# Performance work log

Hardware: AMD Instinct MI355X
Metric: run time of the kernel (lower is better)

## Reference

```python
import jax, jax.numpy as jnp
import numpy as np

B, XD, ZD, XE, H, NH = 8192, 4096, 1024, 64, 128, 4
NUM_STEPS, STEP, NOISE = 10, 0.01, 1.0
EPS = 1e-5


def setup_inputs() -> dict:
    key = jax.random.key(0)
    ks = jax.random.split(key, 16)
    w = lambda k, s: jax.random.normal(k, s, jnp.float32) * 0.02
    inp = {"x": jax.random.normal(ks[0], (B, XD), jnp.float32)}
    inp.update(
        px_W1=w(ks[1], (H, ZD)), px_b1=jnp.zeros(H, jnp.float32),
        px_W2=w(ks[2], (XD, H)), px_b2=jnp.zeros(XD, jnp.float32),
        emb_W=w(ks[3], (XE, XD)), emb_b=jnp.zeros(XE, jnp.float32),
        xp_W=w(ks[4], (H, XE)), xp_b=jnp.zeros(H, jnp.float32),
        zp_W=w(ks[5], (H, ZD)), zp_b=jnp.zeros(H, jnp.float32),
        sa_Wqkv=w(ks[6], (3 * H, H)), sa_bqkv=jnp.zeros(3 * H, jnp.float32),
        sa_Wo=w(ks[7], (H, H)), sa_bo=jnp.zeros(H, jnp.float32),
        ca_Wqkv=w(ks[8], (3 * H, H)), ca_bqkv=jnp.zeros(3 * H, jnp.float32),
        ca_Wo=w(ks[9], (H, H)), ca_bo=jnp.zeros(H, jnp.float32),
        ffn_W1=w(ks[10], (H, H)), ffn_b1=jnp.zeros(H, jnp.float32),
        ffn_W2=w(ks[11], (H, H)), ffn_b2=jnp.zeros(H, jnp.float32),
        ln1_g=jnp.ones(H, jnp.float32), ln1_b=jnp.zeros(H, jnp.float32),
        ln2_g=jnp.ones(H, jnp.float32), ln2_b=jnp.zeros(H, jnp.float32),
        ln3_g=jnp.ones(H, jnp.float32), ln3_b=jnp.zeros(H, jnp.float32),
        out_W=w(ks[12], (1, H)), out_b=jnp.zeros(1, jnp.float32),
    )
    return inp


def _ln(x, g, b):
    m = jnp.mean(x, -1, keepdims=True)
    v = jnp.var(x, -1, keepdims=True)
    return (x - m) * jax.lax.rsqrt(v + EPS) * g + b


def _mha(q, k, v, Wqkv, bqkv, Wo, bo):
    # torch nn.MultiheadAttention math, batch-first layout (B, S, E)
    E = q.shape[-1]
    d = E // NH
    Wq, Wk, Wv = jnp.split(Wqkv, 3, 0)
    bq, bk, bv = jnp.split(bqkv, 3, 0)
    hd = lambda t, W, bb: (t @ W.T + bb).reshape(t.shape[0], t.shape[1], NH, d)
    qh, kh, vh = hd(q, Wq, bq), hd(k, Wk, bk), hd(v, Wv, bv)
    s = jnp.einsum('bqhd,bkhd->bhqk', qh, kh) / jnp.sqrt(jnp.float32(d))
    a = jax.nn.softmax(s, -1)
    o = jnp.einsum('bhqk,bkhd->bqhd', a, vh).reshape(q.shape[0], q.shape[1], E)
    return o @ Wo.T + bo


def _forward(x, px_W1, px_b1, px_W2, px_b2, emb_W, emb_b, xp_W, xp_b, zp_W, zp_b,
             sa_Wqkv, sa_bqkv, sa_Wo, sa_bo, ca_Wqkv, ca_bqkv, ca_Wo, ca_bo,
             ffn_W1, ffn_b1, ffn_W2, ffn_b2, ln1_g, ln1_b, ln2_g, ln2_b,
             ln3_g, ln3_b, out_W, out_b):
    bsz = x.shape[0]
    px = lambda z: jax.nn.relu(z @ px_W1.T + px_b1) @ px_W2.T + px_b2
    grad_fn = jax.grad(lambda z: jnp.sum((px(z) - x) ** 2))
    ks = jax.random.split(jax.random.key(42), NUM_STEPS + 1)
    z0 = jax.random.normal(ks[0], (bsz, ZD), jnp.float32)

    def step(z, k):
        z = z - 0.5 * STEP * grad_fn(z)
        z = z + NOISE * jnp.sqrt(jnp.float32(STEP)) * jax.random.normal(k, z.shape, z.dtype)
        return z, None

    z, _ = jax.lax.scan(step, z0, ks[1:])
    z = jax.lax.stop_gradient(z)  # torch: z.detach()

    x_recon = px(z)                               # (B, XD)
    x_tok = (x @ emb_W.T + emb_b)[:, None, :]     # (B, 1, XE)
    z_lat = z[:, None, :]                         # (B, 1, ZD)
    x_h = x_tok @ xp_W.T + xp_b                   # (B, 1, H)
    z_h = z_lat @ zp_W.T + zp_b                   # (B, 1, H)
    sa = _mha(x_h, x_h, x_h, sa_Wqkv, sa_bqkv, sa_Wo, sa_bo)
    h1 = _ln(x_h + sa, ln1_g, ln1_b)
    ca = _mha(h1, z_h, z_h, ca_Wqkv, ca_bqkv, ca_Wo, ca_bo)
    h2 = _ln(h1 + ca, ln2_g, ln2_b)
    ff = jax.nn.relu(h2 @ ffn_W1.T + ffn_b1) @ ffn_W2.T + ffn_b2
    h3 = _ln(h2 + ff, ln3_g, ln3_b)
    y_pred = h3 @ out_W.T + out_b                 # (B, 1, 1)
    return x_recon, y_pred


def reference(x, px_W1, px_b1, px_W2, px_b2, emb_W, emb_b, xp_W, xp_b, zp_W, zp_b,
              sa_Wqkv, sa_bqkv, sa_Wo, sa_bo, ca_Wqkv, ca_bqkv, ca_Wo, ca_bo,
              ffn_W1, ffn_b1, ffn_W2, ffn_b2, ln1_g, ln1_b, ln2_g, ln2_b,
              ln3_g, ln3_b, out_W, out_b):
    return _forward(x, px_W1, px_b1, px_W2, px_b2, emb_W, emb_b, xp_W, xp_b,
                    zp_W, zp_b, sa_Wqkv, sa_bqkv, sa_Wo, sa_bo, ca_Wqkv,
                    ca_bqkv, ca_Wo, ca_bo, ffn_W1, ffn_b1, ffn_W2, ffn_b2,
                    ln1_g, ln1_b, ln2_g, ln2_b, ln3_g, ln3_b, out_W, out_b)
```

## Files before the change

kernel.cpp:

```cpp
#include <hip/hip_runtime.h>
#include <hip/hip_bf16.h>
#include <cstdint>
#include <cstddef>
#include <cmath>

#define B_     8192
#define XD_    4096
#define ZD_    1024
#define XE_    64
#define H_     128
#define ZN_    (B_*ZD_)

typedef __attribute__((ext_vector_type(8))) short short8_t;
typedef __attribute__((ext_vector_type(4))) float f32x4_t;
#define MFMA16(a,b,c) __builtin_amdgcn_mfma_f32_16x16x32_bf16((a),(b),(c),0,0,0)

__host__ __device__ __forceinline__ uint32_t rotl32_(uint32_t x, int r){
#ifdef __HIP_DEVICE_COMPILE__
  return __builtin_rotateleft32(x, (uint32_t)r);
#else
  return (x<<r)|(x>>(32-r));
#endif
}

__host__ __device__ __forceinline__ void tf2x32(uint32_t k0, uint32_t k1,
                                                uint32_t x0, uint32_t x1,
                                                uint32_t* o0, uint32_t* o1){
  uint32_t k2 = k0 ^ k1 ^ 0x1BD11BDAu;
  x0 += k0; x1 += k1;
  x0 += x1; x1 = rotl32_(x1,13); x1 ^= x0;
  x0 += x1; x1 = rotl32_(x1,15); x1 ^= x0;
  x0 += x1; x1 = rotl32_(x1,26); x1 ^= x0;
  x0 += x1; x1 = rotl32_(x1, 6); x1 ^= x0;
  x0 += k1; x1 += k2 + 1u;
  x0 += x1; x1 = rotl32_(x1,17); x1 ^= x0;
  x0 += x1; x1 = rotl32_(x1,29); x1 ^= x0;
  x0 += x1; x1 = rotl32_(x1,16); x1 ^= x0;
  x0 += x1; x1 = rotl32_(x1,24); x1 ^= x0;
  x0 += k2; x1 += k0 + 2u;
  x0 += x1; x1 = rotl32_(x1,13); x1 ^= x0;
  x0 += x1; x1 = rotl32_(x1,15); x1 ^= x0;
  x0 += x1; x1 = rotl32_(x1,26); x1 ^= x0;
  x0 += x1; x1 = rotl32_(x1, 6); x1 ^= x0;
  x0 += k0; x1 += k1 + 3u;
  x0 += x1; x1 = rotl32_(x1,17); x1 ^= x0;
  x0 += x1; x1 = rotl32_(x1,29); x1 ^= x0;
  x0 += x1; x1 = rotl32_(x1,16); x1 ^= x0;
  x0 += x1; x1 = rotl32_(x1,24); x1 ^= x0;
  x0 += k1; x1 += k2 + 4u;
  x0 += x1; x1 = rotl32_(x1,13); x1 ^= x0;
  x0 += x1; x1 = rotl32_(x1,15); x1 ^= x0;
  x0 += x1; x1 = rotl32_(x1,26); x1 ^= x0;
  x0 += x1; x1 = rotl32_(x1, 6); x1 ^= x0;
  x0 += k2; x1 += k0 + 5u;
  *o0 = x0; *o1 = x1;
}

__device__ __forceinline__ float erfinv_(float x){
  float w = -__logf(fmaf(-x, x, 1.0f));
  float p;
  if (w < 5.0f){
    w -= 2.5f;
    p = 2.81022636e-08f;
    p = fmaf(p, w, 3.43273939e-07f);
    p = fmaf(p, w, -3.5233877e-06f);
    p = fmaf(p, w, -4.39150654e-06f);
    p = fmaf(p, w, 0.00021858087f);
    p = fmaf(p, w, -0.00125372503f);
    p = fmaf(p, w, -0.00417768164f);
    p = fmaf(p, w, 0.246640727f);
    p = fmaf(p, w, 1.50140941f);
  } else {
    w = sqrtf(w) - 3.0f;
    p = -0.000200214257f;
    p = fmaf(p, w, 0.000100950558f);
    p = fmaf(p, w, 0.00134934322f);
    p = fmaf(p, w, -0.00367342844f);
    p = fmaf(p, w, 0.00573950773f);
    p = fmaf(p, w, -0.0076224613f);
    p = fmaf(p, w, 0.00943887047f);
    p = fmaf(p, w, 1.00167406f);
    p = fmaf(p, w, 2.83297682f);
  }
  return p * x;
}

__device__ __forceinline__ float bits_to_normal(uint32_t bits){
  float f = __uint_as_float((bits >> 9) | 0x3f800000u) - 1.0f;
  float u = fmaxf(-0.99999994f, fmaf(f, 2.0f, -0.99999994f));
  return 1.41421356f * erfinv_(u);
}

__device__ __forceinline__ float rng_normal(uint32_t k0, uint32_t k1, uint32_t idx){
  uint32_t o0, o1; tf2x32(k0, k1, 0u, idx, &o0, &o1);
  return bits_to_normal(o0 ^ o1);
}

__device__ __forceinline__ ushort f2bf(float f){
  return __builtin_bit_cast(ushort, __float2bfloat16(f));
}
__device__ __forceinline__ float bf2f(ushort u){ return __uint_as_float(((uint32_t)u) << 16); }

__device__ __forceinline__ void gen8(uint32_t k0, uint32_t k1, uint32_t base, uint4* g){
  union { ushort u[8]; uint4 q; } pk;
  #pragma unroll
  for (int j = 0; j < 8; ++j) pk.u[j] = f2bf(rng_normal(k0,k1,base+(uint32_t)j));
  *g = pk.q;
}

__global__ void k_prepA(const float* __restrict__ saWo, const float* __restrict__ saWqkv,
                        const float* __restrict__ caWo, const float* __restrict__ caWqkv,
                        float* __restrict__ S, float* __restrict__ U){
  int blk = blockIdx.x, tid = threadIdx.x;
  int idx = (blk & 255) * 64 + tid;
  int i = idx >> 7, j = idx & 127;
  if (blk < 256){
    float acc = (i == j) ? 1.0f : 0.0f;
    for (int k = 0; k < H_; ++k) acc += saWo[i*H_ + k] * saWqkv[(2*H_ + k)*H_ + j];
    S[idx] = acc;
  } else {
    float acc = 0.0f;
    for (int k = 0; k < H_; ++k) acc += caWo[i*H_ + k] * caWqkv[(2*H_ + k)*H_ + j];
    U[idx] = acc;
  }
}

__global__ void k_prepB(const float* __restrict__ saWo, const float* __restrict__ sabqkv, const float* __restrict__ sabo,
                        const float* __restrict__ caWo, const float* __restrict__ cabqkv, const float* __restrict__ cabo,
                        const float* __restrict__ W2, const float* __restrict__ pb2,
                        float* __restrict__ s0, float* __restrict__ u0, float* __restrict__ cb,
                        uint32_t* __restrict__ dkeys){
  int blk = blockIdx.x, tid = threadIdx.x;
  if (blk == 0 && tid == 0){
    for (uint32_t i = 0; i < 11; ++i){
      uint32_t a, b; tf2x32(0u, 42u, 0u, i, &a, &b);
      dkeys[2*i] = a; dkeys[2*i+1] = b;
    }
  }
  if (blk < 2){
    int i = blk*64 + tid;
    float acc = sabo[i];
    for (int k = 0; k < H_; ++k) acc += saWo[i*H_ + k] * sabqkv[2*H_ + k];
    s0[i] = acc;
  } else if (blk < 4){
    int i = (blk-2)*64 + tid;
    float acc = cabo[i];
    for (int k = 0; k < H_; ++k) acc += caWo[i*H_ + k] * cabqkv[2*H_ + k];
    u0[i] = acc;
  } else {
    int j = (blk-4)*64 + tid;
    float acc = 0.0f;
    for (int c = 0; c < XD_; ++c) acc += pb2[c] * W2[(size_t)c*H_ + j];
    cb[j] = acc;
  }
}

__global__ void k_prepTR(const float* __restrict__ S, const float* __restrict__ U,
                         const float* __restrict__ xpW, const float* __restrict__ zpW,
                         const float* __restrict__ xpb, const float* __restrict__ zpb,
                         const float* __restrict__ s0, const float* __restrict__ u0,
                         float* __restrict__ T, float* __restrict__ R,
                         float* __restrict__ t0, float* __restrict__ r0v){
  int blk = blockIdx.x, tid = threadIdx.x;
  if (blk < 128){
    int idx = blk*64 + tid;
    int i = idx >> 6, e = idx & 63;
    float acc = 0.0f;
    for (int m = 0; m < H_; ++m) acc += S[i*H_ + m] * xpW[m*XE_ + e];
    T[idx] = acc;
  } else if (blk < 2176){
    int idx = (blk-128)*64 + tid;
    int i = idx >> 10, k = idx & 1023;
    float acc = 0.0f;
    for (int m = 0; m < H_; ++m) acc += U[i*H_ + m] * zpW[(size_t)m*ZD_ + k];
    R[idx] = acc;
  } else if (blk < 2178){
    int i = (blk-2176)*64 + tid;
    float acc = s0[i];
    for (int m = 0; m < H_; ++m) acc += S[i*H_ + m] * xpb[m];
    t0[i] = acc;
  } else {
    int i = (blk-2178)*64 + tid;
    float acc = u0[i];
    for (int m = 0; m < H_; ++m) acc += U[i*H_ + m] * zpb[m];
    r0v[i] = acc;
  }
}

__global__ void k_prepMG_part(const float* __restrict__ W2, const float* __restrict__ W1,
                              const float* __restrict__ R,
                              float* __restrict__ Mpart, float* __restrict__ Gpart){
  int gid = blockIdx.x*256 + threadIdx.x;
  if (gid < 131072){
    int slice = gid >> 14, i = gid & 16383;
    int j1 = i >> 7, j2 = i & 127;
    int c0 = slice*512;
    float acc = 0.0f;
    for (int c = c0; c < c0+512; ++c)
      acc += W2[(size_t)c*H_ + j1] * W2[(size_t)c*H_ + j2];
    Mpart[(size_t)slice*16384 + i] = acc;
  } else {
    int g = gid - 131072;
    int slice = g >> 15, i2 = g & 32767;
    int i = i2 >> 7, k = i2 & 127;
    int m0 = slice*128;
    float acc = 0.0f;
    if (i < 128){
      for (int m = m0; m < m0+128; ++m)
        acc += W1[(size_t)i*ZD_ + m] * W1[(size_t)k*ZD_ + m];
    } else {
      for (int m = m0; m < m0+128; ++m)
        acc += W1[(size_t)k*ZD_ + m] * R[(size_t)(i-128)*ZD_ + m];
    }
    Gpart[(size_t)slice*32768 + i2] = acc;
  }
}

__global__ void k_prepWXT(const float* __restrict__ W2, const float* __restrict__ T,
                          const float* __restrict__ embW, const float* __restrict__ embb,
                          const float* __restrict__ t0,
                          ushort* __restrict__ WXT, float* __restrict__ q0){
  int idx = blockIdx.x*256 + threadIdx.x;
  int j = idx >> 12, c = idx & 4095;
  float v;
  if (j < H_) v = W2[(size_t)c*H_ + j];
  else {
    int i = j - H_;
    float acc = 0.0f;
    for (int e = 0; e < XE_; ++e) acc += T[i*XE_ + e] * embW[(size_t)e*XD_ + c];
    v = acc;
  }
  WXT[idx] = f2bf(v);
  if (idx < H_){
    float acc = t0[idx];
    for (int e = 0; e < XE_; ++e) acc += T[idx*XE_ + e] * embb[e];
    q0[idx] = acc;
  }
}

__global__ void k_conv(const float* __restrict__ W2, const float* __restrict__ W1,
                       const float* __restrict__ R,
                       const float* __restrict__ Mpart, const float* __restrict__ Gpart,
                       ushort* __restrict__ W2bf, ushort* __restrict__ Mbf,
                       ushort* __restrict__ FBT, ushort* __restrict__ GGr){
  int idx = blockIdx.x*256 + threadIdx.x;
  if (idx < 524288) W2bf[idx] = f2bf(W2[idx]);
  else if (idx < 540672){
    int i = idx - 524288;
    float s = 0.0f;
    #pragma unroll
    for (int p = 0; p < 8; ++p) s += Mpart[(size_t)p*16384 + i];
    Mbf[i] = f2bf(2.0f*s);
  } else if (idx < 802816){
    int i = idx - 540672; int j = i >> 10, k = i & 1023;
    FBT[i] = f2bf(j < H_ ? W1[j*ZD_ + k] : R[(size_t)(j-H_)*ZD_ + k]);
  } else {
    int i = idx - 802816;
    float s = 0.0f;
    #pragma unroll
    for (int p = 0; p < 8; ++p) s += Gpart[(size_t)p*32768 + i];
    GGr[i] = f2bf(-0.005f*s);
  }
}

__global__ __launch_bounds__(256) void k_noiseproj(
    const ushort* __restrict__ FBT, const uint32_t* __restrict__ dkeys,
    float* __restrict__ y0c0, ushort* __restrict__ NWR){
  const int t = threadIdx.x, lane = t & 63, w = t >> 6;
  const int l15 = lane & 15, kq8 = (lane >> 4)*8, rq = (lane >> 4)*4;
  const int gwid = blockIdx.x*4 + w;
  const int p = gwid >> 9, mb = gwid & 511;
  const int row0 = mb*16;
  const uint32_t k0 = dkeys[2*p], k1 = dkeys[2*p+1];
  const uint32_t rbase = (uint32_t)(row0 + l15)*1024u + (uint32_t)kq8;
  f32x4_t acc[16] = {};
  #pragma unroll 1
  for (int it = 0; it < 16; ++it){
    const ushort* fb = &FBT[(size_t)l15*ZD_ + it*64 + kq8];
    uint4 br[16];
    #pragma unroll
    for (int cf = 0; cf < 16; ++cf) br[cf] = *(const uint4*)(fb + (size_t)cf*16*ZD_);
    __builtin_amdgcn_sched_barrier(0);
    uint4 g0; gen8(k0, k1, rbase + (uint32_t)(it*64), &g0);
    short8_t a0 = __builtin_bit_cast(short8_t, g0);
    #pragma unroll
    for (int cf = 0; cf < 16; ++cf)
      acc[cf] = MFMA16(a0, __builtin_bit_cast(short8_t, br[cf]), acc[cf]);
    #pragma unroll
    for (int cf = 0; cf < 16; ++cf) br[cf] = *(const uint4*)(fb + (size_t)cf*16*ZD_ + 32);
    __builtin_amdgcn_sched_barrier(0);
    uint4 g1; gen8(k0, k1, rbase + (uint32_t)(it*64 + 32), &g1);
    short8_t a1 = __builtin_bit_cast(short8_t, g1);
    #pragma unroll
    for (int cf = 0; cf < 16; ++cf)
      acc[cf] = MFMA16(a1, __builtin_bit_cast(short8_t, br[cf]), acc[cf]);
  }
  #pragma unroll
  for (int cf = 0; cf < 16; ++cf){
    int col = cf*16 + l15;
    #pragma unroll
    for (int r = 0; r < 4; ++r){
      int row = row0 + rq + r;
      float v = acc[cf][r];
      if (p == 0) y0c0[(size_t)row*256 + col] = v;
      else NWR[(size_t)(p-1)*2097152 + (size_t)row*256 + col] = f2bf(0.1f*v);
    }
  }
}

__global__ __launch_bounds__(256) void k_xpass_mfma(
    const float* __restrict__ x, const ushort* __restrict__ WXT,
    const float* __restrict__ cb, const float* __restrict__ q0,
    float* __restrict__ cneg, float* __restrict__ h1pre){
  __shared__ __align__(16) ushort xt[2][32*72];
  __shared__ __align__(16) ushort bt[2][128*72];
  const int t = threadIdx.x, lane = t & 63, w = t >> 6;
  const int bm = blockIdx.x >> 1, bn = blockIdx.x & 1;
  const int row0 = bm*32, ncol0 = bn*128;
  const int l15 = lane & 15, kq8 = (lane >> 4)*8, rq = (lane >> 4)*4;
  const int rt = w & 1, cb4 = (w >> 1)*4;
  const int xr = t >> 3, xk = (t & 7)*8;
  const int wn = t >> 1, wk = (t & 1)*32;
  f32x4_t acc[4] = {};
  {
    float4 v0 = *(const float4*)&x[(size_t)(row0+xr)*XD_ + xk];
    float4 v1 = *(const float4*)&x[(size_t)(row0+xr)*XD_ + xk + 4];
    union { ushort u[8]; uint4 q; } p;
    p.u[0]=f2bf(v0.x); p.u[1]=f2bf(v0.y); p.u[2]=f2bf(v0.z); p.u[3]=f2bf(v0.w);
    p.u[4]=f2bf(v1.x); p.u[5]=f2bf(v1.y); p.u[6]=f2bf(v1.z); p.u[7]=f2bf(v1.w);
    *(uint4*)&xt[0][xr*72 + xk] = p.q;
    const ushort* s = &WXT[(size_t)(ncol0+wn)*XD_ + wk];
    uint4 b0v=*(const uint4*)s, b1v=*(const uint4*)(s+8), b2v=*(const uint4*)(s+16), b3v=*(const uint4*)(s+24);
    ushort* d = &bt[0][wn*72 + wk];
    *(uint4*)d=b0v; *(uint4*)(d+8)=b1v; *(uint4*)(d+16)=b2v; *(uint4*)(d+24)=b3v;
  }
  float4 xv0, xv1; uint4 wb0, wb1, wb2, wb3;
  {
    xv0 = *(const float4*)&x[(size_t)(row0+xr)*XD_ + 64 + xk];
    xv1 = *(const float4*)&x[(size_t)(row0+xr)*XD_ + 64 + xk + 4];
    const ushort* s = &WXT[(size_t)(ncol0+wn)*XD_ + 64 + wk];
    wb0=*(const uint4*)s; wb1=*(const uint4*)(s+8); wb2=*(const uint4*)(s+16); wb3=*(const uint4*)(s+24);
  }
  #pragma unroll 1
  for (int it = 0; it < 64; ++it){
    __syncthreads();
    if (it < 63){
      union { ushort u[8]; uint4 q; } p;
      p.u[0]=f2bf(xv0.x); p.u[1]=f2bf(xv0.y); p.u[2]=f2bf(xv0.z); p.u[3]=f2bf(xv0.w);
      p.u[4]=f2bf(xv1.x); p.u[5]=f2bf(xv1.y); p.u[6]=f2bf(xv1.z); p.u[7]=f2bf(xv1.w);
      *(uint4*)&xt[(it+1)&1][xr*72 + xk] = p.q;
      ushort* d = &bt[(it+1)&1][wn*72 + wk];
      *(uint4*)d=wb0; *(uint4*)(d+8)=wb1; *(uint4*)(d+16)=wb2; *(uint4*)(d+24)=wb3;
    }
    if (it < 62){
      const int kt = (it+2)*64;
      xv0 = *(const float4*)&x[(size_t)(row0+xr)*XD_ + kt + xk];
      xv1 = *(const float4*)&x[(size_t)(row0+xr)*XD_ + kt + xk + 4];
      const ushort* s = &WXT[(size_t)(ncol0+wn)*XD_ + kt + wk];
      wb0=*(const uint4*)s; wb1=*(const uint4*)(s+8); wb2=*(const uint4*)(s+16); wb3=*(const uint4*)(s+24);
    }
    const ushort* xb = &xt[it&1][(rt*16+l15)*72];
    const ushort* bb = &bt[it&1][0];
    #pragma unroll
    for (int h = 0; h < 2; ++h){
      short8_t a = *(const short8_t*)(xb + h*32 + kq8);
      #pragma unroll
      for (int c = 0; c < 4; ++c){
        short8_t b = *(const short8_t*)(bb + ((cb4+c)*16+l15)*72 + h*32 + kq8);
        acc[c] = MFMA16(a, b, acc[c]);
      }
    }
  }
  #pragma unroll
  for (int c = 0; c < 4; ++c){
    int jl = (cb4+c)*16 + l15;
    #pragma unroll
    for (int r = 0; r < 4; ++r){
      int row = row0 + rt*16 + rq + r;
      float v = acc[c][r];
      if (bn == 0) cneg[(size_t)row*H_ + jl] = 2.0f*(cb[jl] - v);
      else         h1pre[(size_t)row*H_ + jl] = v + q0[jl];
    }
  }
}

__global__ __launch_bounds__(512) void k_lv2(
    const ushort* __restrict__ M2bf, const ushort* __restrict__ GGr,
    const float* __restrict__ y0c0, const ushort* __restrict__ NWR,
    const float* __restrict__ b1, const float* __restrict__ r0v,
    const float* __restrict__ cneg,
    ushort* __restrict__ hfin_bf, float* __restrict__ capre){
  __shared__ __align__(16) ushort abuf[16*136];
  __shared__ __align__(16) ushort glbuf[16*136];
  const int t = threadIdx.x, lane = t & 63, w = t >> 6;
  const int l15 = lane & 15, kq8 = (lane >> 4)*8, rq = (lane >> 4)*4;
  const int b0 = blockIdx.x * 16;
  const int myc = w*16 + l15;
  const int col2 = w*32 + l15;

  f32x4_t acc[2];
  #pragma unroll
  for (int nf = 0; nf < 2; ++nf)
    #pragma unroll
    for (int r = 0; r < 4; ++r)
      acc[nf][r] = y0c0[(size_t)(b0+rq+r)*256 + col2 + nf*16];
  float cn[4];
  #pragma unroll
  for (int r = 0; r < 4; ++r) cn[r] = cneg[(size_t)(b0+rq+r)*H_ + myc];
  float bb2[2];
  bb2[0] = (w < 4) ? b1[col2] : 0.0f;
  bb2[1] = (w < 4) ? b1[col2+16] : 0.0f;
  ushort nx[8];
  #pragma unroll
  for (int nf = 0; nf < 2; ++nf)
    #pragma unroll
    for (int r = 0; r < 4; ++r)
      nx[nf*4+r] = NWR[(size_t)(b0+rq+r)*256 + col2 + nf*16];

  #pragma unroll 1
  for (int s = 0; s < 10; ++s){
    if (w < 4){
      #pragma unroll
      for (int nf = 0; nf < 2; ++nf)
        #pragma unroll
        for (int r = 0; r < 4; ++r)
          abuf[(rq+r)*136 + col2 + nf*16] = f2bf(fmaxf(acc[nf][r] + bb2[nf], 0.0f));
    }
    __syncthreads();
    f32x4_t g2 = {};
    #pragma unroll
    for (int h = 0; h < 4; ++h){
      short8_t a = *(const short8_t*)&abuf[l15*136 + h*32 + kq8];
      short8_t b = *(const short8_t*)&M2bf[(size_t)myc*H_ + h*32 + kq8];
      g2 = MFMA16(a, b, g2);
    }
    #pragma unroll
    for (int r = 0; r < 4; ++r){
      float g = (abuf[(rq+r)*136 + myc] != 0) ? (g2[r] + cn[r]) : 0.0f;
      glbuf[(rq+r)*136 + myc] = f2bf(g);
    }
    __syncthreads();
    #pragma unroll
    for (int nf = 0; nf < 2; ++nf)
      #pragma unroll
      for (int h = 0; h < 4; ++h){
        short8_t a = *(const short8_t*)&glbuf[l15*136 + h*32 + kq8];
        short8_t b = *(const short8_t*)&GGr[(size_t)(col2 + nf*16)*H_ + h*32 + kq8];
        acc[nf] = MFMA16(a, b, acc[nf]);
      }
    #pragma unroll
    for (int nf = 0; nf < 2; ++nf)
      #pragma unroll
      for (int r = 0; r < 4; ++r)
        acc[nf][r] += bf2f(nx[nf*4+r]);
    if (s < 9){
      #pragma unroll
      for (int nf = 0; nf < 2; ++nf)
        #pragma unroll
        for (int r = 0; r < 4; ++r)
          nx[nf*4+r] = NWR[(size_t)(s+1)*2097152 + (size_t)(b0+rq+r)*256 + col2 + nf*16];
    }
    __syncthreads();
  }
  if (w < 4){
    #pragma unroll
    for (int nf = 0; nf < 2; ++nf)
      #pragma unroll
      for (int r = 0; r < 4; ++r)
        hfin_bf[(size_t)(b0+rq+r)*H_ + col2 + nf*16] = f2bf(fmaxf(acc[nf][r] + bb2[nf], 0.0f));
  } else {
    #pragma unroll
    for (int nf = 0; nf < 2; ++nf)
      #pragma unroll
      for (int r = 0; r < 4; ++r)
        capre[(size_t)(b0+rq+r)*H_ + (col2 + nf*16 - 128)] = acc[nf][r] + r0v[col2 + nf*16 - 128];
  }
}

__global__ __launch_bounds__(256) void k_xrecon_mfma(
    const ushort* __restrict__ hfin_bf, const ushort* __restrict__ W2bf,
    const float* __restrict__ b2, float* __restrict__ out){
  __shared__ __align__(16) ushort at[64*136];
  __shared__ __align__(16) ushort bt[128*136];
  const int tid = threadIdx.x, lane = tid & 63, w = tid >> 6;
  const int bm = blockIdx.x >> 5, bn = blockIdx.x & 31;
  const int row0 = bm*64, c0 = bn*128;
  const int l15 = lane & 15, kq8 = (lane >> 4)*8, rq = (lane >> 4)*4;
  { int r = tid >> 2, kq = (tid & 3)*32;
    const ushort* src = &hfin_bf[(size_t)(row0 + r)*H_ + kq];
    #pragma unroll
    for (int i = 0; i < 4; ++i) *(uint4*)&at[r*136 + kq + 8*i] = *(const uint4*)(src + 8*i);
  }
  { int n = tid >> 1, kh = (tid & 1)*64;
    const ushort* src = &W2bf[(size_t)(c0 + n)*H_ + kh];
    #pragma unroll
    for (int i = 0; i < 8; ++i) *(uint4*)&bt[n*136 + kh + 8*i] = *(const uint4*)(src + 8*i);
  }
  __syncthreads();
  f32x4_t acc[8] = {};
  #pragma unroll
  for (int k = 0; k < 4; ++k){
    short8_t a = *(const short8_t*)&at[(w*16 + l15)*136 + k*32 + kq8];
    #pragma unroll
    for (int nf = 0; nf < 8; ++nf){
      short8_t b = *(const short8_t*)&bt[(nf*16 + l15)*136 + k*32 + kq8];
      acc[nf] = MFMA16(a, b, acc[nf]);
    }
  }
  #pragma unroll
  for (int nf = 0; nf < 8; ++nf){
    int c = c0 + nf*16 + l15;
    float bbv = b2[c];
    #pragma unroll
    for (int r = 0; r < 4; ++r){
      int row = row0 + w*16 + rq + r;
      out[(size_t)row*XD_ + c] = acc[nf][r] + bbv;
    }
  }
}

__device__ __forceinline__ float wsum64(float v){
  #pragma unroll
  for (int off = 32; off > 0; off >>= 1) v += __shfl_xor(v, off, 64);
  return v;
}

__global__ __launch_bounds__(256) void k_tail(
    const float* __restrict__ h1pre, const float* __restrict__ capre,
    const float* __restrict__ ln1g, const float* __restrict__ ln1b,
    const float* __restrict__ ln2g, const float* __restrict__ ln2b,
    const float* __restrict__ ln3g, const float* __restrict__ ln3b,
    const float* __restrict__ fW1, const float* __restrict__ fb1,
    const float* __restrict__ fW2, const float* __restrict__ fb2,
    const float* __restrict__ outW, const float* __restrict__ outb,
    float* __restrict__ y){
  __shared__ float sh2[4][128];
  __shared__ float st1[4][128];
  const int tid = threadIdx.x;
  const int w = tid >> 6;
  const int l = tid & 63;
  const int b = blockIdx.x * 4 + w;
  const float* hp = h1pre + (size_t)b * H_;
  const float* cp = capre + (size_t)b * H_;
  float x0 = hp[l], x1 = hp[l+64];
  float m = wsum64(x0 + x1) * (1.0f/128.0f);
  float d0 = x0 - m, d1 = x1 - m;
  float v = wsum64(d0*d0 + d1*d1) * (1.0f/128.0f);
  float rs = rsqrtf(v + 1e-5f);
  float h1a = d0 * rs * ln1g[l]    + ln1b[l];
  float h1b = d1 * rs * ln1g[l+64] + ln1b[l+64];
  x0 = h1a + cp[l]; x1 = h1b + cp[l+64];
  m = wsum64(x0 + x1) * (1.0f/128.0f);
  d0 = x0 - m; d1 = x1 - m;
  v = wsum64(d0*d0 + d1*d1) * (1.0f/128.0f);
  rs = rsqrtf(v + 1e-5f);
  float h2a = d0 * rs * ln2g[l]    + ln2b[l];
  float h2b = d1 * rs * ln2g[l+64] + ln2b[l+64];
  sh2[w][l] = h2a; sh2[w][l+64] = h2b;
  __syncthreads();
  float ta = fb1[l], tb = fb1[l+64];
  #pragma unroll 8
  for (int m4 = 0; m4 < H_; m4 += 4){
    float4 hv = *(const float4*)&sh2[w][m4];
    float4 wa = *(const float4*)&fW1[(size_t)l*H_ + m4];
    float4 wb = *(const float4*)&fW1[(size_t)(l+64)*H_ + m4];
    ta = fmaf(wa.x, hv.x, ta); ta = fmaf(wa.y, hv.y, ta); ta = fmaf(wa.z, hv.z, ta); ta = fmaf(wa.w, hv.w, ta);
    tb = fmaf(wb.x, hv.x, tb); tb = fmaf(wb.y, hv.y, tb); tb = fmaf(wb.z, hv.z, tb); tb = fmaf(wb.w, hv.w, tb);
  }
  ta = fmaxf(ta, 0.0f); tb = fmaxf(tb, 0.0f);
  st1[w][l] = ta; st1[w][l+64] = tb;
  __syncthreads();
  float fa = fb2[l], fbv = fb2[l+64];
  #pragma unroll 8
  for (int m4 = 0; m4 < H_; m4 += 4){
    float4 tv = *(const float4*)&st1[w][m4];
    float4 wa = *(const float4*)&fW2[(size_t)l*H_ + m4];
    float4 wb = *(const float4*)&fW2[(size_t)(l+64)*H_ + m4];
    fa  = fmaf(wa.x, tv.x, fa);  fa  = fmaf(wa.y, tv.y, fa);  fa  = fmaf(wa.z, tv.z, fa);  fa  = fmaf(wa.w, tv.w, fa);
    fbv = fmaf(wb.x, tv.x, fbv); fbv = fmaf(wb.y, tv.y, fbv); fbv = fmaf(wb.z, tv.z, fbv); fbv = fmaf(wb.w, tv.w, fbv);
  }
  x0 = h2a + fa; x1 = h2b + fbv;
  m = wsum64(x0 + x1) * (1.0f/128.0f);
  d0 = x0 - m; d1 = x1 - m;
  v = wsum64(d0*d0 + d1*d1) * (1.0f/128.0f);
  rs = rsqrtf(v + 1e-5f);
  float h3a = d0 * rs * ln3g[l]    + ln3b[l];
  float h3b = d1 * rs * ln3g[l+64] + ln3b[l+64];
  float py = wsum64(outW[l]*h3a + outW[l+64]*h3b);
  if (l == 0) y[b] = py + outb[0];
}

extern "C" void kernel_launch(void* const* d_in, const int* in_sizes, int n_in,
                              void* d_out, int out_size, void* d_ws, size_t ws_size,
                              hipStream_t stream){
  const float* x      = (const float*)d_in[0];
  const float* pxW1   = (const float*)d_in[1];
  const float* pxb1   = (const float*)d_in[2];
  const float* pxW2   = (const float*)d_in[3];
  const float* pxb2   = (const float*)d_in[4];
  const float* embW   = (const float*)d_in[5];
  const float* embb   = (const float*)d_in[6];
  const float* xpW    = (const float*)d_in[7];
  const float* xpb    = (const float*)d_in[8];
  const float* zpW    = (const float*)d_in[9];
  const float* zpb    = (const float*)d_in[10];
  const float* saWqkv = (const float*)d_in[11];
  const float* sabqkv = (const float*)d_in[12];
  const float* saWo   = (const float*)d_in[13];
  const float* sabo   = (const float*)d_in[14];
  const float* caWqkv = (const float*)d_in[15];
  const float* cabqkv = (const float*)d_in[16];
  const float* caWo   = (const float*)d_in[17];
  const float* cabo   = (const float*)d_in[18];
  const float* fW1    = (const float*)d_in[19];
  const float* fb1    = (const float*)d_in[20];
  const float* fW2    = (const float*)d_in[21];
  const float* fb2    = (const float*)d_in[22];
  const float* ln1g   = (const float*)d_in[23];
  const float* ln1b   = (const float*)d_in[24];
  const float* ln2g   = (const float*)d_in[25];
  const float* ln2b   = (const float*)d_in[26];
  const float* ln3g   = (const float*)d_in[27];
  const float* ln3b   = (const float*)d_in[28];
  const float* outW   = (const float*)d_in[29];
  const float* outb   = (const float*)d_in[30];
  (void)in_sizes; (void)n_in; (void)out_size; (void)ws_size;

  float* ws    = (float*)d_ws;
  float* cneg  = ws;
  float* h1pre = cneg + (size_t)B_*H_;
  float* capre = h1pre + (size_t)B_*H_;
  float* Rm    = capre + (size_t)B_*H_;
  float* Sm    = Rm + (size_t)H_*ZD_;
  float* Um    = Sm + H_*H_;
  float* Tm    = Um + H_*H_;
  float* vs0   = Tm + H_*XE_;
  float* vu0   = vs0 + H_;
  float* vt0   = vu0 + H_;
  float* vq0   = vt0 + H_;
  float* vr0   = vq0 + H_;
  float* vcb   = vr0 + H_;
  float* Mpart = vcb + H_;
  float* Gpart = Mpart + 131072;
  uint32_t* dkeys = (uint32_t*)(Gpart + 262144);
  float* y0c0  = (float*)(dkeys + 32);
  ushort* WXT   = (ushort*)(y0c0 + (size_t)B_*256);
  ushort* W2bf  = WXT + (size_t)256*XD_;
  ushort* Mbf   = W2bf + (size_t)XD_*H_;
  ushort* FBT   = Mbf + H_*H_;
  ushort* GGr   = FBT + (size_t)256*ZD_;
  ushort* hfin  = GGr + (size_t)256*H_;
  ushort* NWR   = hfin + (size_t)B_*H_;

  float* xre   = (float*)d_out;
  float* ypred = xre + (size_t)B_*XD_;

  k_prepA   <<<512,  64, 0, stream>>>(saWo, saWqkv, caWo, caWqkv, Sm, Um);
  k_prepB   <<<6,    64, 0, stream>>>(saWo, sabqkv, sabo, caWo, cabqkv, cabo, pxW2, pxb2,
                                      vs0, vu0, vcb, dkeys);
  k_prepTR  <<<2180, 64, 0, stream>>>(Sm, Um, xpW, zpW, xpb, zpb, vs0, vu0, Tm, Rm, vt0, vr0);
  k_prepMG_part <<<1536, 256, 0, stream>>>(pxW2, pxW1, Rm, Mpart, Gpart);
  k_prepWXT <<<4096, 256, 0, stream>>>(pxW2, Tm, embW, embb, vt0, WXT, vq0);
  k_conv    <<<3264, 256, 0, stream>>>(pxW2, pxW1, Rm, Mpart, Gpart, W2bf, Mbf, FBT, GGr);
  k_noiseproj <<<1408, 256, 0, stream>>>(FBT, dkeys, y0c0, NWR);
  k_xpass_mfma <<<512, 256, 0, stream>>>(x, WXT, vcb, vq0, cneg, h1pre);
  k_lv2     <<<512, 512, 0, stream>>>(Mbf, GGr, y0c0, NWR, pxb1, vr0, cneg, hfin, capre);
  k_xrecon_mfma <<<4096, 256, 0, stream>>>(hfin, W2bf, pxb2, xre);
  k_tail    <<<2048, 256, 0, stream>>>(h1pre, capre, ln1g, ln1b, ln2g, ln2b, ln3g, ln3b,
                                       fW1, fb1, fW2, fb2, outW, outb, ypred);
}
```

Before: 874.3 us.

## Merge prep kernels and pre-swizzle FBT into MFMA fragment order for noiseproj

Merges k_prepA with k_prepB, and k_prepMG_part with k_prepWXT, into single launches, removing two kernel launches and their serialization gaps. FBT is now written by k_conv in the exact per-lane MFMA fragment order, so k_noiseproj's B-operand loads become contiguous 16-byte-per-lane accesses instead of strided rows. The permuted layout only works because the noiseproj indexing was changed to match it. Merged kernels run heterogeneous work in one grid, which may imbalance blocks.

```diff
diff --git a/kernel.cpp b/kernel.cpp
--- a/kernel.cpp
+++ b/kernel.cpp
@@ -108,50 +108,51 @@
   *g = pk.q;
 }
 
-__global__ void k_prepA(const float* __restrict__ saWo, const float* __restrict__ saWqkv,
-                        const float* __restrict__ caWo, const float* __restrict__ caWqkv,
-                        float* __restrict__ S, float* __restrict__ U){
+__global__ void k_prepAB(const float* __restrict__ saWo, const float* __restrict__ saWqkv,
+                         const float* __restrict__ caWo, const float* __restrict__ caWqkv,
+                         const float* __restrict__ sabqkv, const float* __restrict__ sabo,
+                         const float* __restrict__ cabqkv, const float* __restrict__ cabo,
+                         const float* __restrict__ W2, const float* __restrict__ pb2,
+                         float* __restrict__ S, float* __restrict__ U,
+                         float* __restrict__ s0, float* __restrict__ u0, float* __restrict__ cb,
+                         uint32_t* __restrict__ dkeys){
   int blk = blockIdx.x, tid = threadIdx.x;
-  int idx = (blk & 255) * 64 + tid;
-  int i = idx >> 7, j = idx & 127;
-  if (blk < 256){
-    float acc = (i == j) ? 1.0f : 0.0f;
-    for (int k = 0; k < H_; ++k) acc += saWo[i*H_ + k] * saWqkv[(2*H_ + k)*H_ + j];
-    S[idx] = acc;
+  if (blk < 512){
+    int idx = (blk & 255) * 64 + tid;
+    int i = idx >> 7, j = idx & 127;
+    if (blk < 256){
+      float acc = (i == j) ? 1.0f : 0.0f;
+      for (int k = 0; k < H_; ++k) acc += saWo[i*H_ + k] * saWqkv[(2*H_ + k)*H_ + j];
+      S[idx] = acc;
+    } else {
+      float acc = 0.0f;
+      for (int k = 0; k < H_; ++k) acc += caWo[i*H_ + k] * caWqkv[(2*H_ + k)*H_ + j];
+      U[idx] = acc;
+    }
   } else {
-    float acc = 0.0f;
-    for (int k = 0; k < H_; ++k) acc += caWo[i*H_ + k] * caWqkv[(2*H_ + k)*H_ + j];
-    U[idx] = acc;
-  }
-}
-
-__global__ void k_prepB(const float* __restrict__ saWo, const float* __restrict__ sabqkv, const float* __restrict__ sabo,
-                        const float* __restrict__ caWo, const float* __restrict__ cabqkv, const float* __restrict__ cabo,
-                        const float* __restrict__ W2, const float* __restrict__ pb2,
-                        float* __restrict__ s0, float* __restrict__ u0, float* __restrict__ cb,
-                        uint32_t* __restrict__ dkeys){
-  int blk = blockIdx.x, tid = threadIdx.x;
-  if (blk == 0 && tid == 0){
-    for (uint32_t i = 0; i < 11; ++i){
-      uint32_t a, b; tf2x32(0u, 42u, 0u, i, &a, &b);
-      dkeys[2*i] = a; dkeys[2*i+1] = b;
-    }
-  }
-  if (blk < 2){
-    int i = blk*64 + tid;
-    float acc = sabo[i];
-    for (int k = 0; k < H_; ++k) acc += saWo[i*H_ + k] * sabqkv[2*H_ + k];
-    s0[i] = acc;
-  } else if (blk < 4){
-    int i = (blk-2)*64 + tid;
-    float acc = cabo[i];
-    for (int k = 0; k < H_; ++k) acc += caWo[i*H_ + k] * cabqkv[2*H_ + k];
-    u0[i] = acc;
-  } else {
-    int j = (blk-4)*64 + tid;
-    float acc = 0.0f;
-    for (int c = 0; c < XD_; ++c) acc += pb2[c] * W2[(size_t)c*H_ + j];
-    cb[j] = acc;
+    int b2 = blk - 512;
+    if (b2 == 0 && tid == 0){
+      for (uint32_t i = 0; i < 11; ++i){
+        uint32_t a, b; tf2x32(0u, 42u, 0u, i, &a, &b);
+        dkeys[2*i] = a; dkeys[2*i+1] = b;
+      }
+    }
+    if (b2 < 2){
+      int i = b2*64 + tid;
+      float acc = sabo[i];
+      for (int k = 0; k < H_; ++k) acc += saWo[i*H_ + k] * sabqkv[2*H_ + k];
+      s0[i] = acc;
+    } else if (b2 < 4){
+      int i = (b2-2)*64 + tid;
+      float acc = cabo[i];
+      for (int k = 0; k < H_; ++k) acc += caWo[i*H_ + k] * cabqkv[2*H_ + k];
+      u0[i] = acc;
+    } else {
+      int j = (b2-4)*64 + tid;
+      float acc = 0.0f;
+      for (int c = 0; c < XD_; ++c) acc += pb2[c] * W2[(size_t)c*H_ + j];
+      cb[j] = acc;
+    }
   }
 }
 
@@ -187,54 +188,54 @@
   }
 }
 
-__global__ void k_prepMG_part(const float* __restrict__ W2, const float* __restrict__ W1,
-                              const float* __restrict__ R,
-                              float* __restrict__ Mpart, float* __restrict__ Gpart){
-  int gid = blockIdx.x*256 + threadIdx.x;
-  if (gid < 131072){
-    int slice = gid >> 14, i = gid & 16383;
-    int j1 = i >> 7, j2 = i & 127;
-    int c0 = slice*512;
-    float acc = 0.0f;
-    for (int c = c0; c < c0+512; ++c)
-      acc += W2[(size_t)c*H_ + j1] * W2[(size_t)c*H_ + j2];
-    Mpart[(size_t)slice*16384 + i] = acc;
+__global__ void k_prepWM(const float* __restrict__ W2, const float* __restrict__ T,
+                         const float* __restrict__ embW, const float* __restrict__ embb,
+                         const float* __restrict__ t0, const float* __restrict__ W1,
+                         const float* __restrict__ R,
+                         ushort* __restrict__ WXT, float* __restrict__ q0,
+                         float* __restrict__ Mpart, float* __restrict__ Gpart){
+  if (blockIdx.x < 4096){
+    int idx = blockIdx.x*256 + threadIdx.x;
+    int j = idx >> 12, c = idx & 4095;
+    float v;
+    if (j < H_) v = W2[(size_t)c*H_ + j];
+    else {
+      int i = j - H_;
+      float acc = 0.0f;
+      for (int e = 0; e < XE_; ++e) acc += T[i*XE_ + e] * embW[(size_t)e*XD_ + c];
+      v = acc;
+    }
+    WXT[idx] = f2bf(v);
+    if (idx < H_){
+      float acc = t0[idx];
+      for (int e = 0; e < XE_; ++e) acc += T[idx*XE_ + e] * embb[e];
+      q0[idx] = acc;
+    }
   } else {
-    int g = gid - 131072;
-    int slice = g >> 15, i2 = g & 32767;
-    int i = i2 >> 7, k = i2 & 127;
-    int m0 = slice*128;
-    float acc = 0.0f;
-    if (i < 128){
-      for (int m = m0; m < m0+128; ++m)
-        acc += W1[(size_t)i*ZD_ + m] * W1[(size_t)k*ZD_ + m];
+    int gid = (blockIdx.x - 4096)*256 + threadIdx.x;
+    if (gid < 131072){
+      int slice = gid >> 14, i = gid & 16383;
+      int j1 = i >> 7, j2 = i & 127;
+      int c0 = slice*512;
+      float acc = 0.0f;
+      for (int c = c0; c < c0+512; ++c)
+        acc += W2[(size_t)c*H_ + j1] * W2[(size_t)c*H_ + j2];
+      Mpart[(size_t)slice*16384 + i] = acc;
     } else {
-      for (int m = m0; m < m0+128; ++m)
-        acc += W1[(size_t)k*ZD_ + m] * R[(size_t)(i-128)*ZD_ + m];
-    }
-    Gpart[(size_t)slice*32768 + i2] = acc;
-  }
-}
-
-__global__ void k_prepWXT(const float* __restrict__ W2, const float* __restrict__ T,
-                          const float* __restrict__ embW, const float* __restrict__ embb,
-                          const float* __restrict__ t0,
-                          ushort* __restrict__ WXT, float* __restrict__ q0){
-  int idx = blockIdx.x*256 + threadIdx.x;
-  int j = idx >> 12, c = idx & 4095;
-  float v;
-  if (j < H_) v = W2[(size_t)c*H_ + j];
-  else {
-    int i = j - H_;
-    float acc = 0.0f;
-    for (int e = 0; e < XE_; ++e) acc += T[i*XE_ + e] * embW[(size_t)e*XD_ + c];
-    v = acc;
-  }
-  WXT[idx] = f2bf(v);
-  if (idx < H_){
-    float acc = t0[idx];
-    for (int e = 0; e < XE_; ++e) acc += T[idx*XE_ + e] * embb[e];
-    q0[idx] = acc;
+      int g = gid - 131072;
+      int slice = g >> 15, i2 = g & 32767;
+      int i = i2 >> 7, k = i2 & 127;
+      int m0 = slice*128;
+      float acc = 0.0f;
+      if (i < 128){
+        for (int m = m0; m < m0+128; ++m)
+          acc += W1[(size_t)i*ZD_ + m] * W1[(size_t)k*ZD_ + m];
+      } else {
+        for (int m = m0; m < m0+128; ++m)
+          acc += W1[(size_t)k*ZD_ + m] * R[(size_t)(i-128)*ZD_ + m];
+      }
+      Gpart[(size_t)slice*32768 + i2] = acc;
+    }
   }
 }
 
@@ -252,8 +253,16 @@
     for (int p = 0; p < 8; ++p) s += Mpart[(size_t)p*16384 + i];
     Mbf[i] = f2bf(2.0f*s);
   } else if (idx < 802816){
-    int i = idx - 540672; int j = i >> 10, k = i & 1023;
-    FBT[i] = f2bf(j < H_ ? W1[j*ZD_ + k] : R[(size_t)(j-H_)*ZD_ + k]);
+    int i = idx - 540672;
+    int j    = i & 7;
+    int lane = (i >> 3) & 63;
+    int hh   = (i >> 9) & 1;
+    int itt  = (i >> 10) & 15;
+    int cf   = i >> 14;
+    int srow = cf*16 + (lane & 15);
+    int scol = itt*64 + hh*32 + ((lane >> 4) << 3) + j;
+    float v = (srow < H_) ? W1[(size_t)srow*ZD_ + scol] : R[(size_t)(srow-H_)*ZD_ + scol];
+    FBT[i] = f2bf(v);
   } else {
     int i = idx - 802816;
     float s = 0.0f;
@@ -267,27 +276,33 @@
     const ushort* __restrict__ FBT, const uint32_t* __restrict__ dkeys,
     float* __restrict__ y0c0, ushort* __restrict__ NWR){
   const int t = threadIdx.x, lane = t & 63, w = t >> 6;
-  const int l15 = lane & 15, kq8 = (lane >> 4)*8, rq = (lane >> 4)*4;
+  const int l15 = lane & 15, rq = (lane >> 4)*4, kq8 = (lane >> 4)*8;
+  (void)kq8;
   const int gwid = blockIdx.x*4 + w;
   const int p = gwid >> 9, mb = gwid & 511;
   const int row0 = mb*16;
   const uint32_t k0 = dkeys[2*p], k1 = dkeys[2*p+1];
-  const uint32_t rbase = (uint32_t)(row0 + l15)*1024u + (uint32_t)kq8;
+  const uint32_t rbase = (uint32_t)(row0 + l15)*1024u + (uint32_t)((lane >> 4)*8);
   f32x4_t acc[16] = {};
   #pragma unroll 1
   for (int it = 0; it < 16; ++it){
-    const ushort* fb = &FBT[(size_t)l15*ZD_ + it*64 + kq8];
     uint4 br[16];
-    #pragma unroll
-    for (int cf = 0; cf < 16; ++cf) br[cf] = *(const uint4*)(fb + (size_t)cf*16*ZD_);
+    {
+      const ushort* fb = FBT + (size_t)(it*2)*512 + lane*8;
+      #pragma unroll
+      for (int cf = 0; cf < 16; ++cf) br[cf] = *(const uint4*)(fb + (size_t)cf*16384);
+    }
     __builtin_amdgcn_sched_barrier(0);
     uint4 g0; gen8(k0, k1, rbase + (uint32_t)(it*64), &g0);
     short8_t a0 = __builtin_bit_cast(short8_t, g0);
     #pragma unroll
     for (int cf = 0; cf < 16; ++cf)
       acc[cf] = MFMA16(a0, __builtin_bit_cast(short8_t, br[cf]), acc[cf]);
-    #pragma unroll
-    for (int cf = 0; cf < 16; ++cf) br[cf] = *(const uint4*)(fb + (size_t)cf*16*ZD_ + 32);
+    {
+      const ushort* fb = FBT + (size_t)(it*2+1)*512 + lane*8;
+      #pragma unroll
+      for (int cf = 0; cf < 16; ++cf) br[cf] = *(const uint4*)(fb + (size_t)cf*16384);
+    }
     __builtin_amdgcn_sched_barrier(0);
     uint4 g1; gen8(k0, k1, rbase + (uint32_t)(it*64 + 32), &g1);
     short8_t a1 = __builtin_bit_cast(short8_t, g1);
@@ -655,12 +670,11 @@
   float* xre   = (float*)d_out;
   float* ypred = xre + (size_t)B_*XD_;
 
-  k_prepA   <<<512,  64, 0, stream>>>(saWo, saWqkv, caWo, caWqkv, Sm, Um);
-  k_prepB   <<<6,    64, 0, stream>>>(saWo, sabqkv, sabo, caWo, cabqkv, cabo, pxW2, pxb2,
-                                      vs0, vu0, vcb, dkeys);
+  k_prepAB  <<<518,  64, 0, stream>>>(saWo, saWqkv, caWo, caWqkv, sabqkv, sabo,
+                                      cabqkv, cabo, pxW2, pxb2, Sm, Um, vs0, vu0, vcb, dkeys);
   k_prepTR  <<<2180, 64, 0, stream>>>(Sm, Um, xpW, zpW, xpb, zpb, vs0, vu0, Tm, Rm, vt0, vr0);
-  k_prepMG_part <<<1536, 256, 0, stream>>>(pxW2, pxW1, Rm, Mpart, Gpart);
-  k_prepWXT <<<4096, 256, 0, stream>>>(pxW2, Tm, embW, embb, vt0, WXT, vq0);
+  k_prepWM  <<<5632, 256, 0, stream>>>(pxW2, Tm, embW, embb, vt0, pxW1, Rm,
+                                       WXT, vq0, Mpart, Gpart);
   k_conv    <<<3264, 256, 0, stream>>>(pxW2, pxW1, Rm, Mpart, Gpart, W2bf, Mbf, FBT, GGr);
   k_noiseproj <<<1408, 256, 0, stream>>>(FBT, dkeys, y0c0, NWR);
   k_xpass_mfma <<<512, 256, 0, stream>>>(x, WXT, vcb, vq0, cneg, h1pre);
```

Measured after the change: 797.9 us. -8.7%, faster.
